# Kernel tuning notes

Measured on AMD Instinct MI355X. Metric: run time of the kernel, lower is better.

## Reference

```python
import jax, jax.numpy as jnp
import numpy as np

N_NODES = 100000
N_EDGES = 3200000
NUM_GRAPHS = 512


def _glorot(key, shape):
    fan_in, fan_out = shape[0], shape[1]
    lim = float(np.sqrt(6.0 / (fan_in + fan_out)))
    return jax.random.uniform(key, shape, jnp.float32, -lim, lim)


def setup_inputs() -> dict:
    key = jax.random.key(0)
    ks = jax.random.split(key, 12)
    x = jax.random.normal(ks[0], (N_NODES, 3), jnp.float32)
    edge_index = jax.random.randint(ks[1], (2, N_EDGES), 0, N_NODES, jnp.int64)
    batch = jnp.sort(jax.random.randint(ks[2], (N_NODES,), 0, NUM_GRAPHS, jnp.int64))
    return {
        'x': x,
        'edge_index': edge_index,
        'batch': batch,
        'W1': _glorot(ks[3], (3, 32)), 'b1': jnp.zeros((32,), jnp.float32),
        'W2': _glorot(ks[4], (32, 64)), 'b2': jnp.zeros((64,), jnp.float32),
        'W3': _glorot(ks[5], (64, 64)), 'b3': jnp.zeros((64,), jnp.float32),
        'lW1': _glorot(ks[6], (64, 32)), 'lb1': jnp.zeros((32,), jnp.float32),
        'lW2': _glorot(ks[7], (32, 5)), 'lb2': jnp.zeros((5,), jnp.float32),
    }


def gcn_conv(x, src, dst, W, b, n):
    # PyG GCNConv: add self-loops, symmetric deg^{-1/2} normalization,
    # linear transform then gather-scale-scatter aggregation.
    loop = jnp.arange(n, dtype=src.dtype)
    s = jnp.concatenate([src, loop])
    d = jnp.concatenate([dst, loop])
    deg = jax.ops.segment_sum(jnp.ones_like(d, dtype=x.dtype), d, num_segments=n)
    dinv = jnp.where(deg > 0, jax.lax.rsqrt(deg), 0.0)
    norm = dinv[s] * dinv[d]  # [E+N]
    h = x @ W                 # [N, out]
    out = jax.ops.segment_sum(h[s] * norm[:, None], d, num_segments=n)
    return out + b


def reference(x, edge_index, batch, W1, b1, W2, b2, W3, b3, lW1, lb1, lW2, lb2):
    src, dst = edge_index[0], edge_index[1]
    n = x.shape[0]
    h = jax.nn.relu(gcn_conv(x, src, dst, W1, b1, n))
    h = jax.nn.relu(gcn_conv(h, src, dst, W2, b2, n))
    h = gcn_conv(h, src, dst, W3, b3, n)
    pooled = jax.ops.segment_sum(h, batch, num_segments=NUM_GRAPHS)  # [G, 64]
    z = jax.nn.relu(pooled @ lW1 + lb1)
    z = z @ lW2 + lb2
    # original applies log_softmax over dim=0 (the graph axis)
    return jax.nn.log_softmax(z, axis=0)
```

## Files before the change

kernel.cpp:

```cpp
#include <hip/hip_runtime.h>
#include <hip/hip_fp16.h>

#define N_GRAPHS 512
#define NB 1563
#define KNODE 64
#define CAP 3072
#define EPW 8192


__global__ void k_part(const int4* __restrict__ src4, const int4* __restrict__ dst4,
                       int* __restrict__ gCnt, unsigned* __restrict__ ebuf, int E4) {
    __shared__ unsigned pos[NB];
    __shared__ int dstc[EPW];
    int t = threadIdx.x;
    int e0 = blockIdx.x * (EPW / 4);
    int cnt4 = E4 - e0 < EPW / 4 ? E4 - e0 : EPW / 4;
    for (int i = t; i < NB; i += 256) pos[i] = 0;
    __syncthreads();
    for (int i = t; i < cnt4; i += 256) {
        int4 d = dst4[e0 + i];
        dstc[4 * i + 0] = d.x; dstc[4 * i + 1] = d.y;
        dstc[4 * i + 2] = d.z; dstc[4 * i + 3] = d.w;
        atomicAdd(&pos[d.x >> 6], 1u);
        atomicAdd(&pos[d.y >> 6], 1u);
        atomicAdd(&pos[d.z >> 6], 1u);
        atomicAdd(&pos[d.w >> 6], 1u);
    }
    __syncthreads();
    for (int b = t; b < NB; b += 256) {
        unsigned c = pos[b];
        unsigned base = c ? (unsigned)atomicAdd(&gCnt[b], (int)c) : 0u;
        pos[b] = (unsigned)b * CAP + base;
    }
    __syncthreads();
    for (int i = t; i < cnt4; i += 256) {
        int4 s = src4[e0 + i];
#pragma unroll
        for (int q = 0; q < 4; ++q) {
            int d = dstc[4 * i + q];
            int sv = q == 0 ? s.x : q == 1 ? s.y : q == 2 ? s.z : s.w;
            int bkt = d >> 6;
            unsigned p = atomicAdd(&pos[bkt], 1u);
            if (p < (unsigned)(bkt + 1) * CAP)
                ebuf[p] = (unsigned)sv | ((unsigned)(d & 63) << 20);
        }
    }
}


__global__ void k_csr(unsigned* __restrict__ ebuf, const int* __restrict__ gCnt,
                      int2* __restrict__ rows, float* __restrict__ dinv, int n) {
    __shared__ unsigned ec[CAP];
    __shared__ int deg[KNODE];
    __shared__ int pfx[KNODE];
    int b = blockIdx.x, t = threadIdx.x;
    int cnt = gCnt[b];
    if (cnt > CAP) cnt = CAP;
    if (t < KNODE) deg[t] = 0;
    __syncthreads();
    unsigned* eb = ebuf + (size_t)b * CAP;
    for (int i = t; i < cnt; i += 256) {
        unsigned p = eb[i];
        ec[i] = p;
        atomicAdd(&deg[p >> 20], 1);
    }
    __syncthreads();
    if (t == 0) {
        int a = 0;
        for (int i = 0; i < KNODE; ++i) { pfx[i] = a; a += deg[i]; }
    }
    __syncthreads();
    if (t < KNODE) {
        int node = b * KNODE + t;
        if (node < n) {
            rows[node] = make_int2(b * CAP + pfx[t], deg[t]);
            dinv[node] = rsqrtf((float)(deg[t] + 1));
        }
    }
    if (t < KNODE) deg[t] = pfx[t];
    __syncthreads();
    for (int i = t; i < cnt; i += 256) {
        unsigned p = ec[i];
        int pp = atomicAdd(&deg[p >> 20], 1);
        eb[pp] = p & 0xFFFFFu;
    }
}


__global__ void k_pre1(const float* __restrict__ x, const float* __restrict__ dinv,
                       float4* __restrict__ ts0, int n) {
    int i = blockIdx.x * 256 + threadIdx.x;
    if (i >= n) return;
    float d = dinv[i];
    ts0[i] = make_float4(d * x[3 * i], d * x[3 * i + 1], d * x[3 * i + 2], 0.f);
}


__global__ void k_agg1(const float4* __restrict__ ts0, const unsigned* __restrict__ esrc,
                       const int2* __restrict__ rows, const float* __restrict__ dinv,
                       float4* __restrict__ o1, int n) {
    int node = blockIdx.x * 256 + threadIdx.x;
    if (node >= n) return;
    int2 rc = rows[node];
    int s0 = rc.x, deg = rc.y;
    float4 a = ts0[node];
    int e = 0;
    for (; e + 4 <= deg; e += 4) {
        unsigned i0 = esrc[s0 + e + 0];
        unsigned i1 = esrc[s0 + e + 1];
        unsigned i2 = esrc[s0 + e + 2];
        unsigned i3 = esrc[s0 + e + 3];
        float4 v0 = ts0[i0], v1 = ts0[i1], v2 = ts0[i2], v3 = ts0[i3];
        a.x += v0.x + v1.x + v2.x + v3.x;
        a.y += v0.y + v1.y + v2.y + v3.y;
        a.z += v0.z + v1.z + v2.z + v3.z;
    }
    for (; e < deg; ++e) {
        float4 v = ts0[esrc[s0 + e]];
        a.x += v.x; a.y += v.y; a.z += v.z;
    }
    float d = dinv[node];
    o1[node] = make_float4(d * a.x, d * a.y, d * a.z, 0.f);
}


__global__ void k_t1(const float4* __restrict__ o1, const float* __restrict__ W1,
                     const float* __restrict__ b1, const float* __restrict__ dinv,
                     uint4* __restrict__ ts1, int n) {
    __shared__ float sW[96];
    __shared__ float sb[32];
    int t = threadIdx.x;
    if (t < 96) sW[t] = W1[t];
    if (t < 32) sb[t] = b1[t];
    __syncthreads();
    int ln = t >> 2, c = t & 3;
    int node = blockIdx.x * 64 + ln;
    if (node >= n) return;
    float4 o = o1[node];
    float d = dinv[node];
    float r[8];
#pragma unroll
    for (int k = 0; k < 8; ++k) {
        int j = c * 8 + k;
        float h = o.x * sW[j] + o.y * sW[32 + j] + o.z * sW[64 + j] + sb[j];
        r[k] = fmaxf(h, 0.f) * d;
    }
    __half2 h0 = __floats2half2_rn(r[0], r[1]);
    __half2 h1 = __floats2half2_rn(r[2], r[3]);
    __half2 h2 = __floats2half2_rn(r[4], r[5]);
    __half2 h3 = __floats2half2_rn(r[6], r[7]);
    uint4 w;
    w.x = *(unsigned*)&h0; w.y = *(unsigned*)&h1;
    w.z = *(unsigned*)&h2; w.w = *(unsigned*)&h3;
    ts1[((size_t)(c >> 1) * n + node) * 2 + (c & 1)] = w;
}


template <int NSLICE>
__global__ void k_aggG(const uint4* __restrict__ ts, const unsigned* __restrict__ ebuf,
                       const int* __restrict__ gCnt, const int2* __restrict__ rows,
                       const float* __restrict__ dinv, uint4* __restrict__ out, int n) {
    const int XPG = 8 / NSLICE;
    __shared__ unsigned eidx[CAP];
    __shared__ int cursor;
    int i = blockIdx.x;
    int xcd = i & 7;
    int slice = xcd % NSLICE;
    int b = (i >> 3) * XPG + xcd / NSLICE;
    if (b >= NB) return;
    int t = threadIdx.x;
    int cnt = gCnt[b];
    if (cnt > CAP) cnt = CAP;
    int bBase = b * CAP;
    const uint4* ebuf4 = (const uint4*)(ebuf + bBase);
    int cnt4 = (cnt + 3) >> 2;
    for (int k = t; k < cnt4; k += 128) ((uint4*)eidx)[k] = ebuf4[k];
    if (t == 0) cursor = 0;
    __syncthreads();

    const uint4* tss = ts + (size_t)slice * n * 2;
    int lane = t & 1;
    for (;;) {
        int my;
        if (lane == 0) my = atomicAdd(&cursor, 1);
        my = __shfl(my, 0, 2);
        if (my >= KNODE) break;
        int node = b * KNODE + my;
        if (node >= n) continue;
        int2 rc = rows[node];
        int ls = rc.x - bBase;
        int deg = rc.y;
        float2 a0, a1, a2, a3;
        {
            uint4 sv = tss[(size_t)node * 2 + lane];
            a0 = __half22float2(*(__half2*)&sv.x);
            a1 = __half22float2(*(__half2*)&sv.y);
            a2 = __half22float2(*(__half2*)&sv.z);
            a3 = __half22float2(*(__half2*)&sv.w);
        }
        int e = 0;
        for (; e + 4 <= deg; e += 4) {
            unsigned s0 = eidx[ls + e + 0];
            unsigned s1 = eidx[ls + e + 1];
            unsigned s2 = eidx[ls + e + 2];
            unsigned s3 = eidx[ls + e + 3];
            uint4 v0 = tss[(size_t)s0 * 2 + lane];
            uint4 v1 = tss[(size_t)s1 * 2 + lane];
            uint4 v2 = tss[(size_t)s2 * 2 + lane];
            uint4 v3 = tss[(size_t)s3 * 2 + lane];
            float2 f;
            f = __half22float2(*(__half2*)&v0.x); a0.x += f.x; a0.y += f.y;
            f = __half22float2(*(__half2*)&v0.y); a1.x += f.x; a1.y += f.y;
            f = __half22float2(*(__half2*)&v0.z); a2.x += f.x; a2.y += f.y;
            f = __half22float2(*(__half2*)&v0.w); a3.x += f.x; a3.y += f.y;
            f = __half22float2(*(__half2*)&v1.x); a0.x += f.x; a0.y += f.y;
            f = __half22float2(*(__half2*)&v1.y); a1.x += f.x; a1.y += f.y;
            f = __half22float2(*(__half2*)&v1.z); a2.x += f.x; a2.y += f.y;
            f = __half22float2(*(__half2*)&v1.w); a3.x += f.x; a3.y += f.y;
            f = __half22float2(*(__half2*)&v2.x); a0.x += f.x; a0.y += f.y;
            f = __half22float2(*(__half2*)&v2.y); a1.x += f.x; a1.y += f.y;
            f = __half22float2(*(__half2*)&v2.z); a2.x += f.x; a2.y += f.y;
            f = __half22float2(*(__half2*)&v2.w); a3.x += f.x; a3.y += f.y;
            f = __half22float2(*(__half2*)&v3.x); a0.x += f.x; a0.y += f.y;
            f = __half22float2(*(__half2*)&v3.y); a1.x += f.x; a1.y += f.y;
            f = __half22float2(*(__half2*)&v3.z); a2.x += f.x; a2.y += f.y;
            f = __half22float2(*(__half2*)&v3.w); a3.x += f.x; a3.y += f.y;
        }
        for (; e < deg; ++e) {
            unsigned s = eidx[ls + e];
            uint4 v = tss[(size_t)s * 2 + lane];
            float2 f;
            f = __half22float2(*(__half2*)&v.x); a0.x += f.x; a0.y += f.y;
            f = __half22float2(*(__half2*)&v.y); a1.x += f.x; a1.y += f.y;
            f = __half22float2(*(__half2*)&v.z); a2.x += f.x; a2.y += f.y;
            f = __half22float2(*(__half2*)&v.w); a3.x += f.x; a3.y += f.y;
        }
        float dd = dinv[node];
        __half2 o0 = __floats2half2_rn(dd * a0.x, dd * a0.y);
        __half2 o1 = __floats2half2_rn(dd * a1.x, dd * a1.y);
        __half2 o2 = __floats2half2_rn(dd * a2.x, dd * a2.y);
        __half2 o3 = __floats2half2_rn(dd * a3.x, dd * a3.y);
        uint4 w;
        w.x = *(unsigned*)&o0; w.y = *(unsigned*)&o1;
        w.z = *(unsigned*)&o2; w.w = *(unsigned*)&o3;
        out[(size_t)node * (NSLICE * 2) + slice * 2 + lane] = w;
    }
}


__global__ void k_t2(const uint4* __restrict__ o2, const float* __restrict__ W2,
                     const float* __restrict__ b2, const float* __restrict__ dinv,
                     uint4* __restrict__ ts2, int n) {
    __shared__ uint4 sO[128];
    __shared__ float sW[32 * 64];
    __shared__ float sb[64];
    int t = threadIdx.x;
    for (int i = t; i < 32 * 64; i += 256) sW[i] = W2[i];
    if (t < 64) sb[t] = b2[t];
    int node0 = blockIdx.x * 32;
    if (t < 128) {
        int nd = node0 + (t >> 2);
        sO[t] = (nd < n) ? o2[(size_t)node0 * 4 + t] : make_uint4(0, 0, 0, 0);
    }
    __syncthreads();
    int ln = t >> 3, c = t & 7;
    int node = node0 + ln;
    if (node >= n) return;
    const __half2* sOh = (const __half2*)sO;
    float acc[8];
#pragma unroll
    for (int k = 0; k < 8; ++k) acc[k] = sb[c * 8 + k];
#pragma unroll
    for (int i2 = 0; i2 < 16; ++i2) {
        float2 av = __half22float2(sOh[ln * 16 + i2]);
        const float* w0 = &sW[(2 * i2) * 64 + c * 8];
        const float* w1 = &sW[(2 * i2 + 1) * 64 + c * 8];
#pragma unroll
        for (int k = 0; k < 8; ++k) acc[k] += av.x * w0[k] + av.y * w1[k];
    }
    float d = dinv[node];
    float r[8];
#pragma unroll
    for (int k = 0; k < 8; ++k) r[k] = fmaxf(acc[k], 0.f) * d;
    __half2 h0 = __floats2half2_rn(r[0], r[1]);
    __half2 h1 = __floats2half2_rn(r[2], r[3]);
    __half2 h2 = __floats2half2_rn(r[4], r[5]);
    __half2 h3 = __floats2half2_rn(r[6], r[7]);
    uint4 w;
    w.x = *(unsigned*)&h0; w.y = *(unsigned*)&h1;
    w.z = *(unsigned*)&h2; w.w = *(unsigned*)&h3;
    ts2[((size_t)(c >> 1) * n + node) * 2 + (c & 1)] = w;
}


__global__ void k_agg3P(const uint4* __restrict__ ts, const unsigned* __restrict__ ebuf,
                        const int* __restrict__ gCnt, const int2* __restrict__ rows,
                        const float* __restrict__ dinv, const int* __restrict__ batch,
                        float* __restrict__ pooledP, float* __restrict__ cntf, int n) {
    const int NSLICE = 4;
    __shared__ unsigned eidx[CAP];
    __shared__ float buf[KNODE][16];
    __shared__ int bat[KNODE];
    __shared__ int cursor;
    int i = blockIdx.x;
    int xcd = i & 7;
    int slice = xcd % NSLICE;
    int b = (i >> 3) * 2 + xcd / NSLICE;
    if (b >= NB) return;
    int t = threadIdx.x;
    int cnt = gCnt[b];
    if (cnt > CAP) cnt = CAP;
    int bBase = b * CAP;
    const uint4* ebuf4 = (const uint4*)(ebuf + bBase);
    int cnt4 = (cnt + 3) >> 2;
    for (int k = t; k < cnt4; k += 128) ((uint4*)eidx)[k] = ebuf4[k];
    if (t < KNODE) {
        int nd = b * KNODE + t;
        bat[t] = (nd < n) ? batch[nd] : -1;
    }
    if (t == 0) cursor = 0;
    __syncthreads();

    const uint4* tss = ts + (size_t)slice * n * 2;
    int lane = t & 1;
    for (;;) {
        int my;
        if (lane == 0) my = atomicAdd(&cursor, 1);
        my = __shfl(my, 0, 2);
        if (my >= KNODE) break;
        int node = b * KNODE + my;
        if (node >= n) {
#pragma unroll
            for (int k = 0; k < 8; ++k) buf[my][lane * 8 + k] = 0.f;
            continue;
        }
        int2 rc = rows[node];
        int ls = rc.x - bBase;
        int deg = rc.y;
        float2 a0, a1, a2, a3;
        {
            uint4 sv = tss[(size_t)node * 2 + lane];
            a0 = __half22float2(*(__half2*)&sv.x);
            a1 = __half22float2(*(__half2*)&sv.y);
            a2 = __half22float2(*(__half2*)&sv.z);
            a3 = __half22float2(*(__half2*)&sv.w);
        }
        int e = 0;
        for (; e + 4 <= deg; e += 4) {
            unsigned s0 = eidx[ls + e + 0];
            unsigned s1 = eidx[ls + e + 1];
            unsigned s2 = eidx[ls + e + 2];
            unsigned s3 = eidx[ls + e + 3];
            uint4 v0 = tss[(size_t)s0 * 2 + lane];
            uint4 v1 = tss[(size_t)s1 * 2 + lane];
            uint4 v2 = tss[(size_t)s2 * 2 + lane];
            uint4 v3 = tss[(size_t)s3 * 2 + lane];
            float2 f;
            f = __half22float2(*(__half2*)&v0.x); a0.x += f.x; a0.y += f.y;
            f = __half22float2(*(__half2*)&v0.y); a1.x += f.x; a1.y += f.y;
            f = __half22float2(*(__half2*)&v0.z); a2.x += f.x; a2.y += f.y;
            f = __half22float2(*(__half2*)&v0.w); a3.x += f.x; a3.y += f.y;
            f = __half22float2(*(__half2*)&v1.x); a0.x += f.x; a0.y += f.y;
            f = __half22float2(*(__half2*)&v1.y); a1.x += f.x; a1.y += f.y;
            f = __half22float2(*(__half2*)&v1.z); a2.x += f.x; a2.y += f.y;
            f = __half22float2(*(__half2*)&v1.w); a3.x += f.x; a3.y += f.y;
            f = __half22float2(*(__half2*)&v2.x); a0.x += f.x; a0.y += f.y;
            f = __half22float2(*(__half2*)&v2.y); a1.x += f.x; a1.y += f.y;
            f = __half22float2(*(__half2*)&v2.z); a2.x += f.x; a2.y += f.y;
            f = __half22float2(*(__half2*)&v2.w); a3.x += f.x; a3.y += f.y;
            f = __half22float2(*(__half2*)&v3.x); a0.x += f.x; a0.y += f.y;
            f = __half22float2(*(__half2*)&v3.y); a1.x += f.x; a1.y += f.y;
            f = __half22float2(*(__half2*)&v3.z); a2.x += f.x; a2.y += f.y;
            f = __half22float2(*(__half2*)&v3.w); a3.x += f.x; a3.y += f.y;
        }
        for (; e < deg; ++e) {
            unsigned s = eidx[ls + e];
            uint4 v = tss[(size_t)s * 2 + lane];
            float2 f;
            f = __half22float2(*(__half2*)&v.x); a0.x += f.x; a0.y += f.y;
            f = __half22float2(*(__half2*)&v.y); a1.x += f.x; a1.y += f.y;
            f = __half22float2(*(__half2*)&v.z); a2.x += f.x; a2.y += f.y;
            f = __half22float2(*(__half2*)&v.w); a3.x += f.x; a3.y += f.y;
        }
        float dd = dinv[node];
        buf[my][lane * 8 + 0] = dd * a0.x; buf[my][lane * 8 + 1] = dd * a0.y;
        buf[my][lane * 8 + 2] = dd * a1.x; buf[my][lane * 8 + 3] = dd * a1.y;
        buf[my][lane * 8 + 4] = dd * a2.x; buf[my][lane * 8 + 5] = dd * a2.y;
        buf[my][lane * 8 + 6] = dd * a3.x; buf[my][lane * 8 + 7] = dd * a3.y;
    }
    __syncthreads();

    if (t < 16) {
        int f = t;
        float acc = 0.f;
        int gcur = bat[0];
        for (int k = 0; k < KNODE; ++k) {
            int g = bat[k];
            if (g < 0) break;
            if (g != gcur) {
                atomicAdd(&pooledP[gcur * 64 + slice * 16 + f], acc);
                acc = 0.f;
                gcur = g;
            }
            acc += buf[k][f];
        }
        if (gcur >= 0) atomicAdd(&pooledP[gcur * 64 + slice * 16 + f], acc);
    } else if (t == 16 && slice == 0) {
        float rc = 0.f;
        int gcur = bat[0];
        for (int k = 0; k < KNODE; ++k) {
            int g = bat[k];
            if (g < 0) break;
            if (g != gcur) {
                atomicAdd(&cntf[gcur], rc);
                rc = 0.f;
                gcur = g;
            }
            rc += 1.f;
        }
        if (gcur >= 0) atomicAdd(&cntf[gcur], rc);
    }
}


#define GPB 4
__global__ void k_z(const float* __restrict__ P, const float* __restrict__ cntf,
                    const float* __restrict__ W3, const float* __restrict__ b3,
                    const float* __restrict__ lW1, const float* __restrict__ lb1,
                    const float* __restrict__ lW2, const float* __restrict__ lb2,
                    float* __restrict__ z) {
    __shared__ float sW3[64 * 64];
    __shared__ float sW1[64 * 32];
    __shared__ float sW2[32 * 5];
    __shared__ float sb3[64], sb1[32], sb2[5];
    __shared__ float sP[GPB][64];
    __shared__ float sH[GPB][64];
    __shared__ float sT[GPB][32];
    int t = threadIdx.x;
    for (int i = t; i < 64 * 64; i += 256) sW3[i] = W3[i];
    for (int i = t; i < 64 * 32; i += 256) sW1[i] = lW1[i];
    for (int i = t; i < 32 * 5; i += 256) sW2[i] = lW2[i];
    if (t < 64) sb3[t] = b3[t];
    if (t < 32) sb1[t] = lb1[t];
    if (t < 5) sb2[t] = lb2[t];
    int g0 = blockIdx.x * GPB;
    for (int i = t; i < GPB * 64; i += 256) sP[i >> 6][i & 63] = P[(size_t)g0 * 64 + i];
    __syncthreads();
    int lg = t >> 6;
    int j = t & 63;
    int g = g0 + lg;
    float cg = cntf[g];
    float a = cg * sb3[j];
#pragma unroll 8
    for (int i = 0; i < 64; ++i) a += sP[lg][i] * sW3[i * 64 + j];
    sH[lg][j] = a;
    __syncthreads();
    if (j < 32) {
        float a2 = sb1[j];
#pragma unroll 8
        for (int i = 0; i < 64; ++i) a2 += sH[lg][i] * sW1[i * 32 + j];
        sT[lg][j] = fmaxf(a2, 0.f);
    }
    __syncthreads();
    if (j < 5) {
        float a3 = sb2[j];
#pragma unroll
        for (int i = 0; i < 32; ++i) a3 += sT[lg][i] * sW2[i * 5 + j];
        z[g * 5 + j] = a3;
    }
}


__global__ void k_lsm(const float* __restrict__ z, float* __restrict__ out) {
    __shared__ float red[512];
    int g = threadIdx.x;
#pragma unroll
    for (int c = 0; c < 5; ++c) {
        float v = z[g * 5 + c];
        red[g] = v;
        __syncthreads();
        for (int off = 256; off > 0; off >>= 1) {
            if (g < off) red[g] = fmaxf(red[g], red[g + off]);
            __syncthreads();
        }
        float m = red[0];
        __syncthreads();
        red[g] = expf(v - m);
        __syncthreads();
        for (int off = 256; off > 0; off >>= 1) {
            if (g < off) red[g] += red[g + off];
            __syncthreads();
        }
        float lse = m + logf(red[0]);
        __syncthreads();
        out[g * 5 + c] = v - lse;
    }
}


extern "C" void kernel_launch(void* const* d_in, const int* in_sizes, int n_in,
                              void* d_out, int out_size, void* d_ws, size_t ws_size,
                              hipStream_t stream) {
    const float* x   = (const float*)d_in[0];
    const int* ei    = (const int*)d_in[1];
    const int* batch = (const int*)d_in[2];
    const float* W1  = (const float*)d_in[3];
    const float* b1  = (const float*)d_in[4];
    const float* W2  = (const float*)d_in[5];
    const float* b2  = (const float*)d_in[6];
    const float* W3  = (const float*)d_in[7];
    const float* b3  = (const float*)d_in[8];
    const float* lW1 = (const float*)d_in[9];
    const float* lb1 = (const float*)d_in[10];
    const float* lW2 = (const float*)d_in[11];
    const float* lb2 = (const float*)d_in[12];

    const int N = in_sizes[0] / 3;
    const int E = in_sizes[1] / 2;
    const int* src = ei;
    const int* dst = ei + E;

    char* ws = (char*)d_ws;
    size_t off = 0;
    auto alloc = [&](size_t bytes) -> void* {
        void* p = ws + off;
        off = (off + bytes + 255) & ~(size_t)255;
        return p;
    };

    int*      gCnt    = (int*)alloc((size_t)NB * 4);
    float*    dinv    = (float*)alloc((size_t)N * 4);
    int2*     rows    = (int2*)alloc((size_t)N * 8);
    unsigned* ebuf    = (unsigned*)alloc((size_t)NB * CAP * 4);
    float4*   ts0     = (float4*)alloc((size_t)N * 16);
    float4*   o1      = (float4*)alloc((size_t)N * 16);
    uint4*    ts1     = (uint4*)alloc((size_t)N * 4 * 16);
    uint4*    o2      = (uint4*)alloc((size_t)N * 4 * 16);
    uint4*    ts2     = (uint4*)alloc((size_t)N * 8 * 16);
    float*    pooledP = (float*)alloc((size_t)N_GRAPHS * 64 * 4);
    float*    cntf    = (float*)alloc((size_t)N_GRAPHS * 4);
    float*    zbuf    = (float*)alloc((size_t)N_GRAPHS * 5 * 4);

    hipMemsetAsync(gCnt, 0, (size_t)NB * 4, stream);
    hipMemsetAsync(pooledP, 0, (size_t)N_GRAPHS * 64 * 4, stream);
    hipMemsetAsync(cntf, 0, (size_t)N_GRAPHS * 4, stream);

    int nPartWg = (E + EPW - 1) / EPW;
    k_part<<<nPartWg, 256, 0, stream>>>((const int4*)src, (const int4*)dst, gCnt, ebuf, E / 4);
    k_csr<<<NB, 256, 0, stream>>>(ebuf, gCnt, rows, dinv, N);

    k_pre1<<<(N + 255) / 256, 256, 0, stream>>>(x, dinv, ts0, N);
    k_agg1<<<(N + 255) / 256, 256, 0, stream>>>(ts0, ebuf, rows, dinv, o1, N);
    k_t1<<<(N + 63) / 64, 256, 0, stream>>>(o1, W1, b1, dinv, ts1, N);

    k_aggG<2><<<8 * ((NB + 3) / 4), 128, 0, stream>>>(ts1, ebuf, gCnt, rows, dinv, o2, N);
    k_t2<<<(N + 31) / 32, 256, 0, stream>>>(o2, W2, b2, dinv, ts2, N);

    k_agg3P<<<8 * ((NB + 1) / 2), 128, 0, stream>>>(ts2, ebuf, gCnt, rows, dinv, batch,
                                                    pooledP, cntf, N);

    k_z<<<N_GRAPHS / GPB, 256, 0, stream>>>(pooledP, cntf, W3, b3, lW1, lb1, lW2, lb2, zbuf);
    k_lsm<<<1, 512, 0, stream>>>(zbuf, (float*)d_out);
}
```

Measured before the change: 264.7 us.

## Widen gather rows to 64B slices and split pooling into separate kernel

Changes the layer-1 and layer-2 transformed feature layouts so each gather fetches a 64-byte row (4 lanes of uint4) instead of a 32-byte one. Layer 2 now runs as one unsliced pass instead of two XCD-mapped slices, and layer 3 uses 2 slices instead of 4. The fused layer-3 aggregate-plus-pool kernel is replaced by an aggregation that writes o3 to memory, followed by a separate pooling kernel over sorted batch ids. The aim is fewer passes over the edge lists and fuller memory transactions. The cost is an extra full-size o3 write and read, an extra launch, and less L2 locality per XCD slice.

```diff
diff --git a/kernel.cpp b/kernel.cpp
--- a/kernel.cpp
+++ b/kernel.cpp
@@ -152,21 +152,25 @@
     uint4 w;
     w.x = *(unsigned*)&h0; w.y = *(unsigned*)&h1;
     w.z = *(unsigned*)&h2; w.w = *(unsigned*)&h3;
-    ts1[((size_t)(c >> 1) * n + node) * 2 + (c & 1)] = w;
+    ts1[(size_t)node * 4 + c] = w;
 }
 
 
 template <int NSLICE>
-__global__ void k_aggG(const uint4* __restrict__ ts, const unsigned* __restrict__ ebuf,
+__global__ void k_aggW(const uint4* __restrict__ ts, const unsigned* __restrict__ ebuf,
                        const int* __restrict__ gCnt, const int2* __restrict__ rows,
                        const float* __restrict__ dinv, uint4* __restrict__ out, int n) {
-    const int XPG = 8 / NSLICE;
     __shared__ unsigned eidx[CAP];
     __shared__ int cursor;
     int i = blockIdx.x;
-    int xcd = i & 7;
-    int slice = xcd % NSLICE;
-    int b = (i >> 3) * XPG + xcd / NSLICE;
+    int b, slice;
+    if (NSLICE == 1) {
+        b = i; slice = 0;
+    } else {
+        int xcd = i & 7;
+        slice = xcd & 1;
+        b = (i >> 3) * 4 + (xcd >> 1);
+    }
     if (b >= NB) return;
     int t = threadIdx.x;
     int cnt = gCnt[b];
@@ -178,12 +182,12 @@
     if (t == 0) cursor = 0;
     __syncthreads();
 
-    const uint4* tss = ts + (size_t)slice * n * 2;
-    int lane = t & 1;
+    const uint4* tss = ts + (size_t)slice * n * 4;
+    int lane = t & 3;
     for (;;) {
         int my;
         if (lane == 0) my = atomicAdd(&cursor, 1);
-        my = __shfl(my, 0, 2);
+        my = __shfl(my, 0, 4);
         if (my >= KNODE) break;
         int node = b * KNODE + my;
         if (node >= n) continue;
@@ -192,7 +196,7 @@
         int deg = rc.y;
         float2 a0, a1, a2, a3;
         {
-            uint4 sv = tss[(size_t)node * 2 + lane];
+            uint4 sv = tss[(size_t)node * 4 + lane];
             a0 = __half22float2(*(__half2*)&sv.x);
             a1 = __half22float2(*(__half2*)&sv.y);
             a2 = __half22float2(*(__half2*)&sv.z);
@@ -204,10 +208,10 @@
             unsigned s1 = eidx[ls + e + 1];
             unsigned s2 = eidx[ls + e + 2];
             unsigned s3 = eidx[ls + e + 3];
-            uint4 v0 = tss[(size_t)s0 * 2 + lane];
-            uint4 v1 = tss[(size_t)s1 * 2 + lane];
-            uint4 v2 = tss[(size_t)s2 * 2 + lane];
-            uint4 v3 = tss[(size_t)s3 * 2 + lane];
+            uint4 v0 = tss[(size_t)s0 * 4 + lane];
+            uint4 v1 = tss[(size_t)s1 * 4 + lane];
+            uint4 v2 = tss[(size_t)s2 * 4 + lane];
+            uint4 v3 = tss[(size_t)s3 * 4 + lane];
             float2 f;
             f = __half22float2(*(__half2*)&v0.x); a0.x += f.x; a0.y += f.y;
             f = __half22float2(*(__half2*)&v0.y); a1.x += f.x; a1.y += f.y;
@@ -228,7 +232,7 @@
         }
         for (; e < deg; ++e) {
             unsigned s = eidx[ls + e];
-            uint4 v = tss[(size_t)s * 2 + lane];
+            uint4 v = tss[(size_t)s * 4 + lane];
             float2 f;
             f = __half22float2(*(__half2*)&v.x); a0.x += f.x; a0.y += f.y;
             f = __half22float2(*(__half2*)&v.y); a1.x += f.x; a1.y += f.y;
@@ -243,7 +247,7 @@
         uint4 w;
         w.x = *(unsigned*)&o0; w.y = *(unsigned*)&o1;
         w.z = *(unsigned*)&o2; w.w = *(unsigned*)&o3;
-        out[(size_t)node * (NSLICE * 2) + slice * 2 + lane] = w;
+        out[(size_t)node * (NSLICE * 4) + slice * 4 + lane] = w;
     }
 }
 
@@ -289,137 +293,39 @@
     uint4 w;
     w.x = *(unsigned*)&h0; w.y = *(unsigned*)&h1;
     w.z = *(unsigned*)&h2; w.w = *(unsigned*)&h3;
-    ts2[((size_t)(c >> 1) * n + node) * 2 + (c & 1)] = w;
-}
-
-
-__global__ void k_agg3P(const uint4* __restrict__ ts, const unsigned* __restrict__ ebuf,
-                        const int* __restrict__ gCnt, const int2* __restrict__ rows,
-                        const float* __restrict__ dinv, const int* __restrict__ batch,
-                        float* __restrict__ pooledP, float* __restrict__ cntf, int n) {
-    const int NSLICE = 4;
-    __shared__ unsigned eidx[CAP];
-    __shared__ float buf[KNODE][16];
-    __shared__ int bat[KNODE];
-    __shared__ int cursor;
-    int i = blockIdx.x;
-    int xcd = i & 7;
-    int slice = xcd % NSLICE;
-    int b = (i >> 3) * 2 + xcd / NSLICE;
-    if (b >= NB) return;
-    int t = threadIdx.x;
-    int cnt = gCnt[b];
-    if (cnt > CAP) cnt = CAP;
-    int bBase = b * CAP;
-    const uint4* ebuf4 = (const uint4*)(ebuf + bBase);
-    int cnt4 = (cnt + 3) >> 2;
-    for (int k = t; k < cnt4; k += 128) ((uint4*)eidx)[k] = ebuf4[k];
-    if (t < KNODE) {
-        int nd = b * KNODE + t;
-        bat[t] = (nd < n) ? batch[nd] : -1;
-    }
-    if (t == 0) cursor = 0;
-    __syncthreads();
-
-    const uint4* tss = ts + (size_t)slice * n * 2;
-    int lane = t & 1;
-    for (;;) {
-        int my;
-        if (lane == 0) my = atomicAdd(&cursor, 1);
-        my = __shfl(my, 0, 2);
-        if (my >= KNODE) break;
-        int node = b * KNODE + my;
-        if (node >= n) {
-#pragma unroll
-            for (int k = 0; k < 8; ++k) buf[my][lane * 8 + k] = 0.f;
-            continue;
-        }
-        int2 rc = rows[node];
-        int ls = rc.x - bBase;
-        int deg = rc.y;
-        float2 a0, a1, a2, a3;
-        {
-            uint4 sv = tss[(size_t)node * 2 + lane];
-            a0 = __half22float2(*(__half2*)&sv.x);
-            a1 = __half22float2(*(__half2*)&sv.y);
-            a2 = __half22float2(*(__half2*)&sv.z);
-            a3 = __half22float2(*(__half2*)&sv.w);
-        }
-        int e = 0;
-        for (; e + 4 <= deg; e += 4) {
-            unsigned s0 = eidx[ls + e + 0];
-            unsigned s1 = eidx[ls + e + 1];
-            unsigned s2 = eidx[ls + e + 2];
-            unsigned s3 = eidx[ls + e + 3];
-            uint4 v0 = tss[(size_t)s0 * 2 + lane];
-            uint4 v1 = tss[(size_t)s1 * 2 + lane];
-            uint4 v2 = tss[(size_t)s2 * 2 + lane];
-            uint4 v3 = tss[(size_t)s3 * 2 + lane];
-            float2 f;
-            f = __half22float2(*(__half2*)&v0.x); a0.x += f.x; a0.y += f.y;
-            f = __half22float2(*(__half2*)&v0.y); a1.x += f.x; a1.y += f.y;
-            f = __half22float2(*(__half2*)&v0.z); a2.x += f.x; a2.y += f.y;
-            f = __half22float2(*(__half2*)&v0.w); a3.x += f.x; a3.y += f.y;
-            f = __half22float2(*(__half2*)&v1.x); a0.x += f.x; a0.y += f.y;
-            f = __half22float2(*(__half2*)&v1.y); a1.x += f.x; a1.y += f.y;
-            f = __half22float2(*(__half2*)&v1.z); a2.x += f.x; a2.y += f.y;
-            f = __half22float2(*(__half2*)&v1.w); a3.x += f.x; a3.y += f.y;
-            f = __half22float2(*(__half2*)&v2.x); a0.x += f.x; a0.y += f.y;
-            f = __half22float2(*(__half2*)&v2.y); a1.x += f.x; a1.y += f.y;
-            f = __half22float2(*(__half2*)&v2.z); a2.x += f.x; a2.y += f.y;
-            f = __half22float2(*(__half2*)&v2.w); a3.x += f.x; a3.y += f.y;
-            f = __half22float2(*(__half2*)&v3.x); a0.x += f.x; a0.y += f.y;
-            f = __half22float2(*(__half2*)&v3.y); a1.x += f.x; a1.y += f.y;
-            f = __half22float2(*(__half2*)&v3.z); a2.x += f.x; a2.y += f.y;
-            f = __half22float2(*(__half2*)&v3.w); a3.x += f.x; a3.y += f.y;
-        }
-        for (; e < deg; ++e) {
-            unsigned s = eidx[ls + e];
-            uint4 v = tss[(size_t)s * 2 + lane];
-            float2 f;
-            f = __half22float2(*(__half2*)&v.x); a0.x += f.x; a0.y += f.y;
-            f = __half22float2(*(__half2*)&v.y); a1.x += f.x; a1.y += f.y;
-            f = __half22float2(*(__half2*)&v.z); a2.x += f.x; a2.y += f.y;
-            f = __half22float2(*(__half2*)&v.w); a3.x += f.x; a3.y += f.y;
-        }
-        float dd = dinv[node];
-        buf[my][lane * 8 + 0] = dd * a0.x; buf[my][lane * 8 + 1] = dd * a0.y;
-        buf[my][lane * 8 + 2] = dd * a1.x; buf[my][lane * 8 + 3] = dd * a1.y;
-        buf[my][lane * 8 + 4] = dd * a2.x; buf[my][lane * 8 + 5] = dd * a2.y;
-        buf[my][lane * 8 + 6] = dd * a3.x; buf[my][lane * 8 + 7] = dd * a3.y;
-    }
-    __syncthreads();
-
-    if (t < 16) {
-        int f = t;
-        float acc = 0.f;
-        int gcur = bat[0];
-        for (int k = 0; k < KNODE; ++k) {
-            int g = bat[k];
-            if (g < 0) break;
-            if (g != gcur) {
-                atomicAdd(&pooledP[gcur * 64 + slice * 16 + f], acc);
-                acc = 0.f;
-                gcur = g;
-            }
-            acc += buf[k][f];
-        }
-        if (gcur >= 0) atomicAdd(&pooledP[gcur * 64 + slice * 16 + f], acc);
-    } else if (t == 16 && slice == 0) {
-        float rc = 0.f;
-        int gcur = bat[0];
-        for (int k = 0; k < KNODE; ++k) {
-            int g = bat[k];
-            if (g < 0) break;
-            if (g != gcur) {
-                atomicAdd(&cntf[gcur], rc);
-                rc = 0.f;
-                gcur = g;
-            }
-            rc += 1.f;
-        }
-        if (gcur >= 0) atomicAdd(&cntf[gcur], rc);
-    }
+    ts2[((size_t)(c >> 2) * n + node) * 4 + (c & 3)] = w;
+}
+
+
+__global__ void k_pool(const __half2* __restrict__ h, const int* __restrict__ batch,
+                       float* __restrict__ pooled, float* __restrict__ cntf, int n) {
+    const int NBK = 32;
+    int lane = threadIdx.x & 31;
+    int sub = threadIdx.x >> 5;
+    int n0 = (blockIdx.x * 8 + sub) * NBK;
+    if (n0 >= n) return;
+    int nend = n0 + NBK < n ? n0 + NBK : n;
+    float2 acc = make_float2(0.f, 0.f);
+    float rc = 0.f;
+    int gcur = batch[n0];
+    for (int i = n0; i < nend; ++i) {
+        int g = batch[i];
+        if (g != gcur) {
+            atomicAdd(&pooled[gcur * 64 + 2 * lane], acc.x);
+            atomicAdd(&pooled[gcur * 64 + 2 * lane + 1], acc.y);
+            if (lane == 0) atomicAdd(&cntf[gcur], rc);
+            acc = make_float2(0.f, 0.f);
+            rc = 0.f;
+            gcur = g;
+        }
+        float2 v = __half22float2(h[(size_t)i * 32 + lane]);
+        acc.x += v.x;
+        acc.y += v.y;
+        rc += 1.f;
+    }
+    atomicAdd(&pooled[gcur * 64 + 2 * lane], acc.x);
+    atomicAdd(&pooled[gcur * 64 + 2 * lane + 1], acc.y);
+    if (lane == 0) atomicAdd(&cntf[gcur], rc);
 }
 
 
@@ -537,6 +443,7 @@
     uint4*    ts1     = (uint4*)alloc((size_t)N * 4 * 16);
     uint4*    o2      = (uint4*)alloc((size_t)N * 4 * 16);
     uint4*    ts2     = (uint4*)alloc((size_t)N * 8 * 16);
+    uint4*    o3      = (uint4*)alloc((size_t)N * 8 * 16);
     float*    pooledP = (float*)alloc((size_t)N_GRAPHS * 64 * 4);
     float*    cntf    = (float*)alloc((size_t)N_GRAPHS * 4);
     float*    zbuf    = (float*)alloc((size_t)N_GRAPHS * 5 * 4);
@@ -553,12 +460,13 @@
     k_agg1<<<(N + 255) / 256, 256, 0, stream>>>(ts0, ebuf, rows, dinv, o1, N);
     k_t1<<<(N + 63) / 64, 256, 0, stream>>>(o1, W1, b1, dinv, ts1, N);
 
-    k_aggG<2><<<8 * ((NB + 3) / 4), 128, 0, stream>>>(ts1, ebuf, gCnt, rows, dinv, o2, N);
+    k_aggW<1><<<NB, 128, 0, stream>>>(ts1, ebuf, gCnt, rows, dinv, o2, N);
     k_t2<<<(N + 31) / 32, 256, 0, stream>>>(o2, W2, b2, dinv, ts2, N);
 
-    k_agg3P<<<8 * ((NB + 1) / 2), 128, 0, stream>>>(ts2, ebuf, gCnt, rows, dinv, batch,
-                                                    pooledP, cntf, N);
-
+    k_aggW<2><<<8 * ((NB + 3) / 4), 128, 0, stream>>>(ts2, ebuf, gCnt, rows, dinv, o3, N);
+
+    k_pool<<<(N + 8 * 32 - 1) / (8 * 32), 256, 0, stream>>>((const __half2*)o3, batch,
+                                                            pooledP, cntf, N);
     k_z<<<N_GRAPHS / GPB, 256, 0, stream>>>(pooledP, cntf, W3, b3, lW1, lb1, lW2, lb2, zbuf);
     k_lsm<<<1, 512, 0, stream>>>(zbuf, (float*)d_out);
 }
```

New measurement: 245.9 us. 1.08x faster.
